# Kernel optimization log

Measured on AMD Instinct MI355X. Metric: run time of the kernel, lower is better.

## Reference

```python
import jax, jax.numpy as jnp
import numpy as np

S = 1024          # tokens (prefill)
DIM = 2560
HEAD_DIM = 128
N_HEADS = 20
N_KV = 5
HPG = N_HEADS // N_KV      # heads per kv group = 4
GS = 128                   # weight-scale group size
THETA = 500000.0
EPS = 1e-05
QKV_OUT = (N_HEADS + 2 * N_KV) * HEAD_DIM  # 3840


def setup_inputs() -> dict:
    key = jax.random.key(0)
    ks = jax.random.split(key, 7)
    x = jax.random.normal(ks[0], (S, DIM), jnp.float32)
    # unpacked int2 (ternary) weights, stored as float for the reference math
    w_qkv = jax.random.randint(ks[1], (QKV_OUT, DIM), -1, 2).astype(jnp.float32)
    ws_qkv = jax.random.uniform(ks[2], (QKV_OUT, DIM // GS), jnp.float32, 0.01, 0.05)
    w_o = jax.random.randint(ks[3], (DIM, N_HEADS * HEAD_DIM), -1, 2).astype(jnp.float32)
    ws_o = jax.random.uniform(ks[4], (DIM, N_HEADS * HEAD_DIM // GS), jnp.float32, 0.01, 0.05)
    q_norm_w = 1.0 + 0.02 * jax.random.normal(ks[5], (HEAD_DIM,), jnp.float32)
    k_norm_w = 1.0 + 0.02 * jax.random.normal(ks[6], (HEAD_DIM,), jnp.float32)
    return {"x": x, "w_qkv": w_qkv, "ws_qkv": ws_qkv, "w_o": w_o, "ws_o": ws_o,
            "q_norm_w": q_norm_w, "k_norm_w": k_norm_w}


def _quant_act(x):
    # per-token symmetric int8 quant: s = 127 / max|x| (clamped)
    s = 127.0 / jnp.clip(jnp.max(jnp.abs(x), axis=-1, keepdims=True), 1e-05, None)
    q = jnp.clip(jnp.round(x * s), -128.0, 127.0)
    return q, s


def _bitlinear(x, w, ws):
    # int8 activation x int2 weight GEMM with per-(out,group) dequant scales
    q, s = _quant_act(x)
    w_dq = w * jnp.repeat(ws, GS, axis=1)        # [out, in]
    return (q @ w_dq.T) / s


def _rmsnorm(x, w):
    return x * jax.lax.rsqrt(jnp.mean(x * x, axis=-1, keepdims=True) + EPS) * w


def _rope(x, cos, sin):
    # x: [S, ..., d]; cos/sin: [S, d//2], interleaved-pair (llama) convention
    d2 = x.shape[-1] // 2
    shape = (x.shape[0],) + (1,) * (x.ndim - 2) + (d2,)
    c = cos.reshape(shape)
    s = sin.reshape(shape)
    xr = x.reshape(x.shape[:-1] + (d2, 2))
    x0, x1 = xr[..., 0], xr[..., 1]
    out = jnp.stack([x0 * c - x1 * s, x0 * s + x1 * c], axis=-1)
    return out.reshape(x.shape)


def reference(x, w_qkv, ws_qkv, w_o, ws_o, q_norm_w, k_norm_w):
    qkv = _bitlinear(x, w_qkv, ws_qkv)                       # [S, 3840]
    q_size = N_HEADS * HEAD_DIM
    k_size = N_KV * HEAD_DIM
    xq = qkv[:, :q_size].reshape(S, N_KV, HPG, HEAD_DIM)     # [S, g, h, d]
    xk = qkv[:, q_size:q_size + k_size].reshape(S, N_KV, HEAD_DIM)
    xv = qkv[:, q_size + k_size:].reshape(S, N_KV, HEAD_DIM)
    xq = _rmsnorm(xq, q_norm_w)
    xk = _rmsnorm(xk, k_norm_w)
    # RoPE (prefill: positions 0..S-1)
    pos = jnp.arange(S, dtype=jnp.float32)
    inv_freq = THETA ** (-jnp.arange(0, HEAD_DIM, 2, dtype=jnp.float32) / HEAD_DIM)
    ang = pos[:, None] * inv_freq[None, :]                   # [S, d/2]
    cos, sin = jnp.cos(ang), jnp.sin(ang)
    xq = _rope(xq, cos, sin)
    xk = _rope(xk, cos, sin)
    # GQA causal flash-attention math
    scale = HEAD_DIM ** -0.5
    scores = jnp.einsum('sghd,tgd->ghst', xq, xk) * scale    # [g, h, S, S]
    causal = jnp.tril(jnp.ones((S, S), bool))
    scores = jnp.where(causal, scores, -1e30)
    attn = jax.nn.softmax(scores, axis=-1)
    out = jnp.einsum('ghst,tgd->sghd', attn, xv).reshape(S, N_HEADS * HEAD_DIM)
    return _bitlinear(out, w_o, ws_o)                        # [S, DIM]
```

## Files before the change

### kernel.cpp

```cpp
#include <hip/hip_runtime.h>
#include <hip/hip_bf16.h>
#include <cstdint>
#include <math.h>

#define SEQ 1024
#define DIM 2560
#define HD 128
#define NH 20
#define NKV 5
#define QKV_OUT 3840
#define GS 128

typedef __bf16 bf16;
typedef __bf16 bf16x4 __attribute__((ext_vector_type(4)));
typedef __bf16 bf16x8 __attribute__((ext_vector_type(8)));
typedef float f32x4 __attribute__((ext_vector_type(4)));

__global__ __launch_bounds__(256) void fused_pre(
    const float* __restrict__ x, bf16* __restrict__ act, float* __restrict__ rs,
    const float* __restrict__ w1, const float* __restrict__ ws1, bf16* __restrict__ o1,
    const float* __restrict__ w2, const float* __restrict__ ws2, bf16* __restrict__ o2,
    long n1_4, long total4) {
  const int tid = threadIdx.x;
  if (blockIdx.x < SEQ) {
    const int row = blockIdx.x;
    const float* xr = x + (size_t)row * DIM;
    float m = 0.f;
    for (int i = tid; i < DIM; i += 256) m = fmaxf(m, fabsf(xr[i]));
    for (int off = 32; off; off >>= 1) m = fmaxf(m, __shfl_xor(m, off));
    __shared__ float red[4];
    __shared__ float s_bc;
    if ((tid & 63) == 0) red[tid >> 6] = m;
    __syncthreads();
    if (tid == 0) {
      float mm = fmaxf(fmaxf(red[0], red[1]), fmaxf(red[2], red[3]));
      mm = fmaxf(mm, 1e-5f);
      s_bc = 127.f / mm;
      rs[row] = mm / 127.f;
    }
    __syncthreads();
    const float s = s_bc;
    bf16* ar = act + (size_t)row * DIM;
    for (int i = tid; i < DIM; i += 256) {
      float q = rintf(xr[i] * s);
      q = fminf(fmaxf(q, -128.f), 127.f);
      ar[i] = (bf16)q;
    }
  } else {
    long i = (long)(blockIdx.x - SEQ) * 256 + tid;
    if (i >= total4) return;
    const float* w; const float* ws; bf16* o; long e;
    if (i < n1_4) { w = w1; ws = ws1; o = o1; e = i * 4; }
    else          { w = w2; ws = ws2; o = o2; e = (i - n1_4) * 4; }
    int row = (int)(e / DIM);
    int k = (int)(e % DIM);
    float sc = ws[(size_t)row * (DIM / GS) + (k / GS)];
    float4 wv = *(const float4*)(w + e);
    bf16x4 ov;
    ov[0] = (bf16)(wv.x * sc);
    ov[1] = (bf16)(wv.y * sc);
    ov[2] = (bf16)(wv.z * sc);
    ov[3] = (bf16)(wv.w * sc);
    *(bf16x4*)(o + e) = ov;
  }
}

__device__ __forceinline__ void gload_lds16(const bf16* g, bf16* l) {
  __builtin_amdgcn_global_load_lds(
      (const __attribute__((address_space(1))) void*)g,
      (__attribute__((address_space(3))) void*)l, 16, 0, 0);
}

template <int BM, int BN>
__global__ __launch_bounds__(256) void gemm_pipe(
    const bf16* __restrict__ A, const bf16* __restrict__ B,
    const float* __restrict__ rs, float* __restrict__ C,
    int N, int K, int Kh, size_t part_stride, int ND, int NN) {
  constexpr int MI = BM / 32;
  constexpr int NW = BN / 32;
  constexpr int APASS = BM / 32;
  constexpr int BPASS = BN / 32;
  __shared__ bf16 As[2][BM * 64];
  __shared__ bf16 Bs[2][BN * 64];
  const int b = (int)blockIdx.x;
  const int mtile = b / ND;
  const int nz = b % ND;
  const int ntile = nz % NN;
  const int z = nz / NN;
  const int tid = threadIdx.x;
  const int w = tid >> 6, l = tid & 63;
  const int row0 = mtile * BM;
  const int col0 = ntile * BN;
  const int wm = (w >> 1) * (BM / 2), wn = (w & 1) * (BN / 2);
  const int lcol = l & 15, quad = l >> 4;
  const int sr = l >> 3, sg = l & 7;
  const bf16* Ag = A + (size_t)row0 * K + (size_t)z * Kh;
  const bf16* Bg = B + (size_t)col0 * K + (size_t)z * Kh;

  f32x4 acc[MI][NW] = {};

#define STAGE_AB(buf, k0)                                                      \
  {                                                                            \
    _Pragma("unroll") for (int i = 0; i < APASS; ++i) {                        \
      int rb = w * (BM / 4) + i * 8;                                           \
      int r = rb + sr;                                                         \
      gload_lds16(Ag + (size_t)r * K + (k0) + ((sg ^ (r & 7)) * 8),            \
                  &As[buf][rb * 64]);                                          \
    }                                                                          \
    _Pragma("unroll") for (int i = 0; i < BPASS; ++i) {                        \
      int rb = w * (BN / 4) + i * 8;                                           \
      int r = rb + sr;                                                         \
      gload_lds16(Bg + (size_t)r * K + (k0) + ((sg ^ (r & 7)) * 8),            \
                  &Bs[buf][rb * 64]);                                          \
    }                                                                          \
  }

  STAGE_AB(0, 0)
  __syncthreads();

  int buf = 0;
  for (int k0 = 0; k0 < Kh; k0 += 64) {
    if (k0 + 64 < Kh) STAGE_AB(buf ^ 1, k0 + 64)
#pragma unroll
    for (int ks = 0; ks < 2; ++ks) {
      bf16x8 af[MI], bff[NW];
#pragma unroll
      for (int mi = 0; mi < MI; ++mi) {
        int R = wm + mi * 16 + lcol;
        af[mi] = *(const bf16x8*)(&As[buf][R * 64 + (((ks * 4 + quad) ^ (R & 7)) * 8)]);
      }
#pragma unroll
      for (int ni = 0; ni < NW; ++ni) {
        int R = wn + ni * 16 + lcol;
        bff[ni] = *(const bf16x8*)(&Bs[buf][R * 64 + (((ks * 4 + quad) ^ (R & 7)) * 8)]);
      }
#pragma unroll
      for (int mi = 0; mi < MI; ++mi)
#pragma unroll
        for (int ni = 0; ni < NW; ++ni)
          acc[mi][ni] = __builtin_amdgcn_mfma_f32_16x16x32_bf16(
              af[mi], bff[ni], acc[mi][ni], 0, 0, 0);
    }
    __syncthreads();
    buf ^= 1;
  }
#undef STAGE_AB

  float* Cp = C + (size_t)z * part_stride;
#pragma unroll
  for (int mi = 0; mi < MI; ++mi) {
#pragma unroll
    for (int ni = 0; ni < NW; ++ni) {
      int col = col0 + wn + ni * 16 + lcol;
#pragma unroll
      for (int r = 0; r < 4; ++r) {
        int row = row0 + wm + mi * 16 + quad * 4 + r;
        Cp[(size_t)row * N + col] = acc[mi][ni][r] * rs[row];
      }
    }
  }
}

__global__ __launch_bounds__(256) void fused_post(
    const float* __restrict__ qkvA, const float* __restrict__ qkvB,
    const float* __restrict__ qw, const float* __restrict__ kw,
    bf16* __restrict__ Qo, bf16* __restrict__ Ko, bf16* __restrict__ Vt) {
  __shared__ bf16 Ls[64 * 137];
  const int bx = (int)blockIdx.x;
  const int tid = threadIdx.x;
  if (bx < 6400) {
    const int wave = tid >> 6, i = tid & 63;
    const int u = bx * 4 + wave;
    const int t = u & 1023, h = u >> 10;
    const size_t off = (h < NH)
        ? (size_t)t * QKV_OUT + h * HD
        : (size_t)t * QKV_OUT + 2560 + (h - NH) * HD;
    const float* s1 = qkvA + off;
    const float* s2 = qkvB + off;
    float x0 = s1[2 * i] + s2[2 * i];
    float x1 = s1[2 * i + 1] + s2[2 * i + 1];
    float ss = x0 * x0 + x1 * x1;
    for (int off2 = 1; off2 < 64; off2 <<= 1) ss += __shfl_xor(ss, off2);
    float r = rsqrtf(ss * (1.f / 128.f) + 1e-5f);
    const float* wv = (h < NH) ? qw : kw;
    float y0 = x0 * r * wv[2 * i];
    float y1 = x1 * r * wv[2 * i + 1];
    float inv_freq = powf(500000.f, -(float)(2 * i) * (1.f / 128.f));
    float ang = (float)t * inv_freq;
    float sn, cs;
    sincosf(ang, &sn, &cs);
    float o0 = y0 * cs - y1 * sn;
    float o1 = y0 * sn + y1 * cs;
    if (h < NH) {
      bf16* dst = Qo + ((size_t)t * NH + h) * HD + 2 * i;
      dst[0] = (bf16)o0; dst[1] = (bf16)o1;
    } else {
      bf16* dst = Ko + ((size_t)(h - NH) * SEQ + t) * HD + 2 * i;
      dst[0] = (bf16)o0; dst[1] = (bf16)o1;
    }
  } else {
    const int b2 = bx - 6400;
    const int t0 = (b2 & 15) * 64, g = b2 >> 4;
    {
      const int tl = tid >> 4;
      const int d0 = (tid & 15) * 8;
#pragma unroll
      for (int pass = 0; pass < 4; ++pass) {
        int t = pass * 16 + tl;
        size_t off = (size_t)(t0 + t) * QKV_OUT + 3200 + g * HD + d0;
        float4 a = *(const float4*)(qkvA + off);
        float4 b = *(const float4*)(qkvA + off + 4);
        float4 a2 = *(const float4*)(qkvB + off);
        float4 b2v = *(const float4*)(qkvB + off + 4);
        bf16* dst = Ls + t * 137 + d0;
        dst[0] = (bf16)(a.x + a2.x); dst[1] = (bf16)(a.y + a2.y);
        dst[2] = (bf16)(a.z + a2.z); dst[3] = (bf16)(a.w + a2.w);
        dst[4] = (bf16)(b.x + b2v.x); dst[5] = (bf16)(b.y + b2v.y);
        dst[6] = (bf16)(b.z + b2v.z); dst[7] = (bf16)(b.w + b2v.w);
      }
    }
    __syncthreads();
    {
      const int dl = tid >> 3;
      const int tl0 = (tid & 7) * 8;
#pragma unroll
      for (int pass = 0; pass < 4; ++pass) {
        int d = pass * 32 + dl;
        bf16x8 v;
#pragma unroll
        for (int j = 0; j < 8; ++j) v[j] = Ls[(tl0 + j) * 137 + d];
        *(bf16x8*)(Vt + ((size_t)g * HD + d) * SEQ + t0 + tl0) = v;
      }
    }
  }
}

__global__ __launch_bounds__(256, 1) void attn_mfma(
    const bf16* __restrict__ Qb, const bf16* __restrict__ Kb,
    const bf16* __restrict__ Vt, float* __restrict__ Op,
    float* __restrict__ ml) {
  const int p = (int)blockIdx.x;
  int qb, c;
  if (p < 24)      { qb = 31 - p / 3;            c = p % 3; }
  else if (p < 48) { int r = p - 24; qb = 23 - (r >> 1); c = r & 1; }
  else             { qb = 59 - p;                c = 0; }
  const int hp = blockIdx.y;
  const int tid = threadIdx.x;
  const int wave = tid >> 6, lane = tid & 63;
  const int H = (hp >> 1) * 4 + (hp & 1) * 2 + (wave >> 1);
  const int g = H >> 2;
  const int qcol = lane & 15, quad = lane >> 4;
  const int q_tok = qb * 32 + (wave & 1) * 16 + qcol;
  const float scale = 0.08838834764831843f;

  __shared__ bf16 Ks[2][64 * 128];
  __shared__ bf16 Vs[2][128 * 64];

  const bf16* kbase = Kb + (size_t)g * SEQ * HD;
  const bf16* vbase = Vt + (size_t)g * HD * SEQ;

  bf16x8 qf[4];
  {
    const bf16* qp = Qb + ((size_t)q_tok * NH + H) * HD + quad * 8;
#pragma unroll
    for (int kc = 0; kc < 4; ++kc) qf[kc] = *(const bf16x8*)(qp + kc * 32);
  }

  float m_i = -1e30f, l_i = 0.f;
  f32x4 o_acc[8] = {};
  const int kt0 = c * 6;
  int kt_max = kt0 + 5;
  {
    int ktg = (qb * 32 + 31) >> 6;
    if (ktg < kt_max) kt_max = ktg;
  }

  const int k_r = lane >> 4, k_g = lane & 15;
  const int v_r = lane >> 3, v_g = lane & 7;

#define STAGE(buf, key0)                                                       \
  {                                                                            \
    _Pragma("unroll") for (int p2 = 0; p2 < 4; ++p2) {                         \
      int r0 = wave * 16 + p2 * 4;                                             \
      int r = r0 + k_r;                                                        \
      gload_lds16(kbase + (size_t)((key0) + r) * HD + ((k_g ^ (r & 15)) * 8),  \
                  &Ks[buf][r0 * 128]);                                         \
    }                                                                          \
    _Pragma("unroll") for (int p2 = 0; p2 < 4; ++p2) {                         \
      int r0 = wave * 32 + p2 * 8;                                             \
      int r = r0 + v_r;                                                        \
      gload_lds16(vbase + (size_t)r * SEQ + (key0) + ((v_g ^ (r & 7)) * 8),    \
                  &Vs[buf][r0 * 64]);                                          \
    }                                                                          \
  }

  STAGE(0, kt0 * 64)

  for (int kt = kt0; kt <= kt_max; ++kt) {
    const int key0 = kt * 64;
    __syncthreads();
    if (kt < kt_max) STAGE((kt + 1) & 1, key0 + 64)
    const bf16* Kt = Ks[kt & 1];
    const bf16* Vtile = Vs[kt & 1];

    bf16x8 kf[4][4];
#pragma unroll
    for (int mg = 0; mg < 4; ++mg) {
      const int R = mg * 16 + qcol;
      const bf16* krow = Kt + R * 128;
#pragma unroll
      for (int kc = 0; kc < 4; ++kc)
        kf[mg][kc] = *(const bf16x8*)(krow + (((kc * 4 + quad) ^ (R & 15)) * 8));
    }
    f32x4 s[4];
#pragma unroll
    for (int mg = 0; mg < 4; ++mg) {
      f32x4 acc = {0.f, 0.f, 0.f, 0.f};
#pragma unroll
      for (int kc = 0; kc < 4; ++kc)
        acc = __builtin_amdgcn_mfma_f32_16x16x32_bf16(kf[mg][kc], qf[kc], acc, 0, 0, 0);
      s[mg] = acc;
    }

    bf16x8 vf[8][2];
#pragma unroll
    for (int mg2 = 0; mg2 < 8; ++mg2) {
      const int R = mg2 * 16 + qcol;
      const bf16* vrow = Vtile + R * 64;
#pragma unroll
      for (int cc = 0; cc < 2; ++cc) {
        int g8a = cc * 8 + quad;
        int g8b = cc * 8 + 4 + quad;
        bf16x4 v0 = *(const bf16x4*)(vrow + ((g8a >> 1) ^ (R & 7)) * 8 + (g8a & 1) * 4);
        bf16x4 v1 = *(const bf16x4*)(vrow + ((g8b >> 1) ^ (R & 7)) * 8 + (g8b & 1) * 4);
#pragma unroll
        for (int j = 0; j < 4; ++j) { vf[mg2][cc][j] = v0[j]; vf[mg2][cc][j + 4] = v1[j]; }
      }
    }

    float mt = -1e30f;
#pragma unroll
    for (int mg = 0; mg < 4; ++mg)
#pragma unroll
      for (int r = 0; r < 4; ++r) {
        int key = key0 + mg * 16 + quad * 4 + r;
        float v = (key <= q_tok) ? s[mg][r] * scale : -1e30f;
        s[mg][r] = v;
        mt = fmaxf(mt, v);
      }
    mt = fmaxf(mt, __shfl_xor(mt, 16));
    mt = fmaxf(mt, __shfl_xor(mt, 32));
    float mnew = fmaxf(m_i, mt);
    float alpha = __expf(m_i - mnew);
    float ps = 0.f;
#pragma unroll
    for (int mg = 0; mg < 4; ++mg)
#pragma unroll
      for (int r = 0; r < 4; ++r) {
        float pv = __expf(s[mg][r] - mnew);
        s[mg][r] = pv;
        ps += pv;
      }
    ps += __shfl_xor(ps, 16);
    ps += __shfl_xor(ps, 32);
    l_i = l_i * alpha + ps;
    m_i = mnew;
#pragma unroll
    for (int mg2 = 0; mg2 < 8; ++mg2)
#pragma unroll
      for (int r = 0; r < 4; ++r) o_acc[mg2][r] *= alpha;

    bf16x8 pb[2];
#pragma unroll
    for (int cc = 0; cc < 2; ++cc)
#pragma unroll
      for (int j = 0; j < 8; ++j)
        pb[cc][j] = (bf16)s[cc * 2 + (j >> 2)][j & 3];

#pragma unroll
    for (int mg2 = 0; mg2 < 8; ++mg2) {
      f32x4 acc = o_acc[mg2];
#pragma unroll
      for (int cc = 0; cc < 2; ++cc)
        acc = __builtin_amdgcn_mfma_f32_16x16x32_bf16(vf[mg2][cc], pb[cc], acc, 0, 0, 0);
      o_acc[mg2] = acc;
    }
  }
#undef STAGE

  float* op = Op + ((size_t)c * SEQ + q_tok) * DIM + (size_t)H * HD + quad * 4;
#pragma unroll
  for (int mg2 = 0; mg2 < 8; ++mg2)
    *(f32x4*)(op + mg2 * 16) = o_acc[mg2];
  if (lane < 16) {
    size_t mloff = (((size_t)c * SEQ + q_tok) * NH + H) * 2;
    ml[mloff] = m_i;
    ml[mloff + 1] = l_i;
  }
}

__global__ __launch_bounds__(256) void merge_quant(
    const float* __restrict__ Op, const float* __restrict__ ml,
    bf16* __restrict__ act, float* __restrict__ rs) {
  const int t = blockIdx.x;
  const int tid = threadIdx.x;
  const int nc = (((t | 31) >> 6) / 6) + 1;
  __shared__ float sw[3][NH];
  __shared__ float red[4];
  __shared__ float s_bc;
  if (tid < NH) {
    const size_t base = ((size_t)t * NH + tid) * 2;
    const size_t cs = (size_t)SEQ * NH * 2;
    float m0 = ml[base], l0 = ml[base + 1];
    float m1 = 0.f, l1 = 0.f, m2 = 0.f, l2 = 0.f;
    float M = m0;
    if (nc > 1) { m1 = ml[base + cs];     l1 = ml[base + cs + 1];     M = fmaxf(M, m1); }
    if (nc > 2) { m2 = ml[base + 2 * cs]; l2 = ml[base + 2 * cs + 1]; M = fmaxf(M, m2); }
    float w0 = __expf(m0 - M), w1 = 0.f, w2 = 0.f;
    float L = w0 * l0;
    if (nc > 1) { w1 = __expf(m1 - M); L += w1 * l1; }
    if (nc > 2) { w2 = __expf(m2 - M); L += w2 * l2; }
    const float invL = 1.f / L;
    sw[0][tid] = w0 * invL;
    sw[1][tid] = w1 * invL;
    sw[2][tid] = w2 * invL;
  }
  __syncthreads();
  float vals[10];
  float amax = 0.f;
  const float* ob = Op + (size_t)t * DIM;
  const size_t cs = (size_t)SEQ * DIM;
#pragma unroll
  for (int j = 0; j < 10; ++j) {
    int d = j * 256 + tid;
    int h = d >> 7;
    float v = ob[d] * sw[0][h];
    if (nc > 1) v += ob[d + cs] * sw[1][h];
    if (nc > 2) v += ob[d + 2 * cs] * sw[2][h];
    vals[j] = v;
    amax = fmaxf(amax, fabsf(v));
  }
  for (int off = 32; off; off >>= 1) amax = fmaxf(amax, __shfl_xor(amax, off));
  if ((tid & 63) == 0) red[tid >> 6] = amax;
  __syncthreads();
  if (tid == 0) {
    float mm = fmaxf(fmaxf(red[0], red[1]), fmaxf(red[2], red[3]));
    mm = fmaxf(mm, 1e-5f);
    s_bc = 127.f / mm;
    rs[t] = mm / 127.f;
  }
  __syncthreads();
  const float s = s_bc;
  bf16* ar = act + (size_t)t * DIM;
#pragma unroll
  for (int j = 0; j < 10; ++j) {
    float q = rintf(vals[j] * s);
    q = fminf(fmaxf(q, -128.f), 127.f);
    ar[j * 256 + tid] = (bf16)q;
  }
}

extern "C" void kernel_launch(void* const* d_in, const int* in_sizes, int n_in,
                              void* d_out, int out_size, void* d_ws, size_t ws_size,
                              hipStream_t stream) {
  const float* x      = (const float*)d_in[0];
  const float* w_qkv  = (const float*)d_in[1];
  const float* ws_qkv = (const float*)d_in[2];
  const float* w_o    = (const float*)d_in[3];
  const float* ws_o   = (const float*)d_in[4];
  const float* qnw    = (const float*)d_in[5];
  const float* knw    = (const float*)d_in[6];
  float* out = (float*)d_out;

  char* p = (char*)d_ws;
  bf16*  act1 = (bf16*)p;  p += (size_t)SEQ * DIM * 2;
  float* rs1  = (float*)p; p += 4096;
  bf16*  wqdq = (bf16*)p;  p += (size_t)QKV_OUT * DIM * 2;
  bf16*  wodq = (bf16*)p;  p += (size_t)DIM * DIM * 2;
  float* qkvA = (float*)p; p += (size_t)SEQ * QKV_OUT * 4;
  float* qkvB = (float*)p; p += (size_t)SEQ * QKV_OUT * 4;
  bf16*  Qb   = (bf16*)p;  p += (size_t)SEQ * NH * HD * 2;
  bf16*  Kb   = (bf16*)p;  p += (size_t)NKV * SEQ * HD * 2;
  bf16*  Vt   = (bf16*)p;  p += (size_t)NKV * HD * SEQ * 2;
  bf16*  act2 = (bf16*)p;  p += (size_t)SEQ * DIM * 2;
  float* rs2  = (float*)p; p += 4096;

  float* Opart = qkvA;
  float* mlbuf = (float*)act1;

  {
    long n1_4 = (long)QKV_OUT * DIM / 4;
    long total4 = n1_4 + (long)DIM * DIM / 4;
    int dq_blocks = (int)((total4 + 255) / 256);
    fused_pre<<<SEQ + dq_blocks, 256, 0, stream>>>(
        x, act1, rs1, w_qkv, ws_qkv, wqdq, w_o, ws_o, wodq, n1_4, total4);
  }
  gemm_pipe<128, 128><<<480, 256, 0, stream>>>(
      act1, wqdq, rs1, qkvA, QKV_OUT, DIM, DIM / 2, (size_t)SEQ * QKV_OUT, 60, 30);
  fused_post<<<6480, 256, 0, stream>>>(qkvA, qkvB, qnw, knw, Qb, Kb, Vt);
  attn_mfma<<<dim3(60, 10), 256, 0, stream>>>(Qb, Kb, Vt, Opart, mlbuf);
  merge_quant<<<SEQ, 256, 0, stream>>>(Opart, mlbuf, act2, rs2);
  gemm_pipe<64, 64><<<640, 256, 0, stream>>>(
      act2, wodq, rs2, out, DIM, DIM, DIM, 0, 40, 40);
}
```

Before: 226.1 us.

## Overlap w_o dequant with attention and precompute RoPE table

```diff
diff --git a/kernel.cpp b/kernel.cpp
--- a/kernel.cpp
+++ b/kernel.cpp
@@ -19,8 +19,7 @@
 __global__ __launch_bounds__(256) void fused_pre(
     const float* __restrict__ x, bf16* __restrict__ act, float* __restrict__ rs,
     const float* __restrict__ w1, const float* __restrict__ ws1, bf16* __restrict__ o1,
-    const float* __restrict__ w2, const float* __restrict__ ws2, bf16* __restrict__ o2,
-    long n1_4, long total4) {
+    float* __restrict__ rope, long n1_4) {
   const int tid = threadIdx.x;
   if (blockIdx.x < SEQ) {
     const int row = blockIdx.x;
@@ -48,20 +47,29 @@
     }
   } else {
     long i = (long)(blockIdx.x - SEQ) * 256 + tid;
-    if (i >= total4) return;
-    const float* w; const float* ws; bf16* o; long e;
-    if (i < n1_4) { w = w1; ws = ws1; o = o1; e = i * 4; }
-    else          { w = w2; ws = ws2; o = o2; e = (i - n1_4) * 4; }
-    int row = (int)(e / DIM);
-    int k = (int)(e % DIM);
-    float sc = ws[(size_t)row * (DIM / GS) + (k / GS)];
-    float4 wv = *(const float4*)(w + e);
-    bf16x4 ov;
-    ov[0] = (bf16)(wv.x * sc);
-    ov[1] = (bf16)(wv.y * sc);
-    ov[2] = (bf16)(wv.z * sc);
-    ov[3] = (bf16)(wv.w * sc);
-    *(bf16x4*)(o + e) = ov;
+    if (i < n1_4) {
+      long e = i * 4;
+      int row = (int)(e / DIM);
+      int k = (int)(e % DIM);
+      float sc = ws1[(size_t)row * (DIM / GS) + (k / GS)];
+      float4 wv = *(const float4*)(w1 + e);
+      bf16x4 ov;
+      ov[0] = (bf16)(wv.x * sc);
+      ov[1] = (bf16)(wv.y * sc);
+      ov[2] = (bf16)(wv.z * sc);
+      ov[3] = (bf16)(wv.w * sc);
+      *(bf16x4*)(o1 + e) = ov;
+    } else {
+      long u = i - n1_4;
+      if (u >= (long)SEQ * 64) return;
+      int t = (int)(u >> 6), fi = (int)(u & 63);
+      float inv_freq = powf(500000.f, -(float)(2 * fi) * (1.f / 128.f));
+      float ang = (float)t * inv_freq;
+      float sn, cs;
+      sincosf(ang, &sn, &cs);
+      rope[u * 2] = cs;
+      rope[u * 2 + 1] = sn;
+    }
   }
 }
 
@@ -164,6 +172,7 @@
 __global__ __launch_bounds__(256) void fused_post(
     const float* __restrict__ qkvA, const float* __restrict__ qkvB,
     const float* __restrict__ qw, const float* __restrict__ kw,
+    const float* __restrict__ rope,
     bf16* __restrict__ Qo, bf16* __restrict__ Ko, bf16* __restrict__ Vt) {
   __shared__ bf16 Ls[64 * 137];
   const int bx = (int)blockIdx.x;
@@ -177,18 +186,18 @@
         : (size_t)t * QKV_OUT + 2560 + (h - NH) * HD;
     const float* s1 = qkvA + off;
     const float* s2 = qkvB + off;
-    float x0 = s1[2 * i] + s2[2 * i];
-    float x1 = s1[2 * i + 1] + s2[2 * i + 1];
+    float2 xa = *(const float2*)(s1 + 2 * i);
+    float2 xb = *(const float2*)(s2 + 2 * i);
+    float x0 = xa.x + xb.x;
+    float x1 = xa.y + xb.y;
     float ss = x0 * x0 + x1 * x1;
     for (int off2 = 1; off2 < 64; off2 <<= 1) ss += __shfl_xor(ss, off2);
     float r = rsqrtf(ss * (1.f / 128.f) + 1e-5f);
     const float* wv = (h < NH) ? qw : kw;
     float y0 = x0 * r * wv[2 * i];
     float y1 = x1 * r * wv[2 * i + 1];
-    float inv_freq = powf(500000.f, -(float)(2 * i) * (1.f / 128.f));
-    float ang = (float)t * inv_freq;
-    float sn, cs;
-    sincosf(ang, &sn, &cs);
+    float2 csn = *(const float2*)(rope + ((size_t)t * 64 + i) * 2);
+    float cs = csn.x, sn = csn.y;
     float o0 = y0 * cs - y1 * sn;
     float o1 = y0 * sn + y1 * cs;
     if (h < NH) {
@@ -238,14 +247,36 @@
 __global__ __launch_bounds__(256, 1) void attn_mfma(
     const bf16* __restrict__ Qb, const bf16* __restrict__ Kb,
     const bf16* __restrict__ Vt, float* __restrict__ Op,
-    float* __restrict__ ml) {
-  const int p = (int)blockIdx.x;
+    float* __restrict__ ml,
+    const float* __restrict__ w2, const float* __restrict__ ws2,
+    bf16* __restrict__ o2) {
+  const int bxi = (int)blockIdx.x;
+  const int tid = threadIdx.x;
+  if (bxi >= 600) {
+    const long b2 = bxi - 600;
+    const long base4 = b2 * 1024 + tid;
+#pragma unroll
+    for (int it = 0; it < 4; ++it) {
+      long e = (base4 + it * 256) * 4;
+      int row = (int)(e / DIM);
+      int k = (int)(e % DIM);
+      float sc = ws2[(size_t)row * (DIM / GS) + (k / GS)];
+      float4 wv = *(const float4*)(w2 + e);
+      bf16x4 ov;
+      ov[0] = (bf16)(wv.x * sc);
+      ov[1] = (bf16)(wv.y * sc);
+      ov[2] = (bf16)(wv.z * sc);
+      ov[3] = (bf16)(wv.w * sc);
+      *(bf16x4*)(o2 + e) = ov;
+    }
+    return;
+  }
+  const int p = bxi % 60;
+  const int hp = bxi / 60;
   int qb, c;
   if (p < 24)      { qb = 31 - p / 3;            c = p % 3; }
   else if (p < 48) { int r = p - 24; qb = 23 - (r >> 1); c = r & 1; }
   else             { qb = 59 - p;                c = 0; }
-  const int hp = blockIdx.y;
-  const int tid = threadIdx.x;
   const int wave = tid >> 6, lane = tid & 63;
   const int H = (hp >> 1) * 4 + (hp & 1) * 2 + (wave >> 1);
   const int g = H >> 2;
@@ -484,21 +515,21 @@
   bf16*  Vt   = (bf16*)p;  p += (size_t)NKV * HD * SEQ * 2;
   bf16*  act2 = (bf16*)p;  p += (size_t)SEQ * DIM * 2;
   float* rs2  = (float*)p; p += 4096;
-
-  float* Opart = qkvA;
-  float* mlbuf = (float*)act1;
+  float* rope = (float*)p; p += (size_t)SEQ * 64 * 2 * 4;
+  float* Opart = (float*)p; p += (size_t)3 * SEQ * DIM * 4;
+  float* mlbuf = (float*)p; p += (size_t)3 * SEQ * NH * 2 * 4;
 
   {
     long n1_4 = (long)QKV_OUT * DIM / 4;
-    long total4 = n1_4 + (long)DIM * DIM / 4;
-    int dq_blocks = (int)((total4 + 255) / 256);
-    fused_pre<<<SEQ + dq_blocks, 256, 0, stream>>>(
-        x, act1, rs1, w_qkv, ws_qkv, wqdq, w_o, ws_o, wodq, n1_4, total4);
+    int dq_blocks = (int)((n1_4 + 255) / 256);
+    int rope_blocks = (SEQ * 64 + 255) / 256;
+    fused_pre<<<SEQ + dq_blocks + rope_blocks, 256, 0, stream>>>(
+        x, act1, rs1, w_qkv, ws_qkv, wqdq, rope, n1_4);
   }
   gemm_pipe<128, 128><<<480, 256, 0, stream>>>(
       act1, wqdq, rs1, qkvA, QKV_OUT, DIM, DIM / 2, (size_t)SEQ * QKV_OUT, 60, 30);
-  fused_post<<<6480, 256, 0, stream>>>(qkvA, qkvB, qnw, knw, Qb, Kb, Vt);
-  attn_mfma<<<dim3(60, 10), 256, 0, stream>>>(Qb, Kb, Vt, Opart, mlbuf);
+  fused_post<<<6480, 256, 0, stream>>>(qkvA, qkvB, qnw, knw, rope, Qb, Kb, Vt);
+  attn_mfma<<<2200, 256, 0, stream>>>(Qb, Kb, Vt, Opart, mlbuf, w_o, ws_o, wodq);
   merge_quant<<<SEQ, 256, 0, stream>>>(Opart, mlbuf, act2, rs2);
   gemm_pipe<64, 64><<<640, 256, 0, stream>>>(
       act2, wodq, rs2, out, DIM, DIM, DIM, 0, 40, 40);
```

Result: faster. 217.7 us (median of 2 runs) (-3.7%).
